# Optimization experiments

Hardware: AMD Instinct MI355X
Metric: run time of the kernel (lower is better)

The kernel has to match this reference:

```python
import jax, jax.numpy as jnp
import numpy as np
from jax import lax

EPS = 1e-5
NBIT = 127.0  # 8-bit symmetric: 2^(8-1)-1

def ste_round(x):
    return x + lax.stop_gradient(jnp.round(x) - x)

def quant_act(x, rng_max):
    # symmetric fake-quant of activations with learned per-cluster range
    s = rng_max / NBIT
    xq = jnp.clip(ste_round(x / s), -NBIT, NBIT) * s
    return xq, s

def fold_bn(w, gamma, beta, mean, var):
    std = jnp.sqrt(var + EPS)
    scale = gamma / std
    w_f = w * scale[:, None, None, None]
    b_f = beta - mean * scale
    return w_f, b_f

def quant_weight(w):
    # per-output-channel symmetric quant
    s = jnp.max(jnp.abs(w), axis=(1, 2, 3), keepdims=True) / NBIT
    wq = jnp.clip(ste_round(w / s), -NBIT, NBIT) * s
    return wq, s.reshape(-1)

def conv(x, w, stride=1, groups=1, pad=0):
    return lax.conv_general_dilated(
        x, w, window_strides=(stride, stride),
        padding=((pad, pad), (pad, pad)),
        dimension_numbers=('NCHW', 'OIHW', 'NCHW'),
        feature_group_count=groups)

def setup_inputs() -> dict:
    key = jax.random.key(0)
    ks = jax.random.split(key, 24)
    B, Cin, H, W = 64, 96, 28, 28
    Cmid, Cout, NC = 576, 96, 4
    d = {}
    d['x'] = jax.random.normal(ks[0], (B, Cin, H, W), dtype=jnp.float32)
    # conv1: 1x1 expansion
    d['w1'] = jax.random.normal(ks[1], (Cmid, Cin, 1, 1), jnp.float32) * 0.1
    d['g1'] = jax.random.uniform(ks[2], (Cmid,), minval=0.5, maxval=1.5)
    d['b1'] = jax.random.normal(ks[3], (Cmid,)) * 0.1
    d['m1'] = jax.random.normal(ks[4], (Cmid,)) * 0.1
    d['v1'] = jax.random.uniform(ks[5], (Cmid,), minval=0.5, maxval=1.5)
    # conv2: 3x3 depthwise
    d['w2'] = jax.random.normal(ks[6], (Cmid, 1, 3, 3), jnp.float32) * 0.1
    d['g2'] = jax.random.uniform(ks[7], (Cmid,), minval=0.5, maxval=1.5)
    d['b2'] = jax.random.normal(ks[8], (Cmid,)) * 0.1
    d['m2'] = jax.random.normal(ks[9], (Cmid,)) * 0.1
    d['v2'] = jax.random.uniform(ks[10], (Cmid,), minval=0.5, maxval=1.5)
    # conv3: 1x1 projection
    d['w3'] = jax.random.normal(ks[11], (Cout, Cmid, 1, 1), jnp.float32) * 0.1
    d['g3'] = jax.random.uniform(ks[12], (Cout,), minval=0.5, maxval=1.5)
    d['b3'] = jax.random.normal(ks[13], (Cout,)) * 0.1
    d['m3'] = jax.random.normal(ks[14], (Cout,)) * 0.1
    d['v3'] = jax.random.uniform(ks[15], (Cout,), minval=0.5, maxval=1.5)
    # per-cluster learned activation ranges for the 4 QuantAct modules
    d['r0'] = jax.random.uniform(ks[16], (NC,), minval=2.0, maxval=8.0)
    d['r1'] = jax.random.uniform(ks[17], (NC,), minval=2.0, maxval=8.0)
    d['r2'] = jax.random.uniform(ks[18], (NC,), minval=2.0, maxval=8.0)
    d['r3'] = jax.random.uniform(ks[19], (NC,), minval=2.0, maxval=8.0)
    d['cluster'] = 2
    return d

def reference(x, w1, g1, b1, m1, v1, w2, g2, b2, m2, v2,
              w3, g3, b3, m3, v3, r0, r1, r2, r3, cluster):
    identity = x  # residual path (in==out, stride==1)
    # QuantAct -> conv1 (BN-folded, per-channel quant) -> ReLU6
    xq, s0 = quant_act(x, r0[cluster])
    w1f, bf1 = fold_bn(w1, g1, b1, m1, v1)
    w1q, ws1 = quant_weight(w1f)
    y = conv(xq, w1q) + bf1[None, :, None, None]
    y = jnp.clip(y, 0.0, 6.0)
    # QuantAct1 -> depthwise conv2 -> ReLU6
    yq, s1 = quant_act(y, r1[cluster])
    w2f, bf2 = fold_bn(w2, g2, b2, m2, v2)
    w2q, ws2 = quant_weight(w2f)
    y = conv(yq, w2q, stride=1, groups=w2.shape[0], pad=1) + bf2[None, :, None, None]
    y = jnp.clip(y, 0.0, 6.0)
    # QuantAct2 -> conv3 projection
    yq, s2 = quant_act(y, r2[cluster])
    w3f, bf3 = fold_bn(w3, g3, b3, m3, v3)
    w3q, ws3 = quant_weight(w3f)
    y = conv(yq, w3q) + bf3[None, :, None, None]
    # residual add, then int32 requant
    y = y + identity
    out, s3 = quant_act(y, r3[cluster])
    return out, s3
```

## Files before the change

kernel.cpp:

```cpp
#include <hip/hip_runtime.h>
#include <cstdint>
#include <cstddef>

typedef int   v4i __attribute__((ext_vector_type(4)));
typedef float v4f __attribute__((ext_vector_type(4)));
typedef unsigned int u32;

constexpr int B_   = 64;
constexpr int CIN  = 96;
constexpr int P_   = 784;
constexpr int CMID = 576;
constexpr int COUT = 96;
constexpr int NOUT = B_ * COUT * P_;
constexpr float NBITF = 127.0f;
constexpr float EPSF  = 1e-5f;
constexpr float MAGICF = 12582912.0f;
constexpr int   BIASI  = 0x4B400000;

constexpr int XB4 = 13 * 8 * 64;

__device__ __forceinline__ int dot3(u32 a, u32 w, int acc) {
#if __has_builtin(__builtin_amdgcn_sdot4)
    return __builtin_amdgcn_sdot4((int)a, (int)w, acc, false);
#else
    return acc + (int)(signed char)(a)        * (int)(signed char)(w)
               + (int)(signed char)(a >> 8)   * (int)(signed char)(w >> 8)
               + (int)(signed char)(a >> 16)  * (int)(signed char)(w >> 16);
#endif
}

__device__ __forceinline__ void tr4(u32 S0, u32 S1, u32 S2, u32 S3, u32 O[4]) {
    u32 u01 = __builtin_amdgcn_perm(S1, S0, 0x05010400u);
    u32 u23 = __builtin_amdgcn_perm(S3, S2, 0x05010400u);
    u32 v01 = __builtin_amdgcn_perm(S1, S0, 0x07030602u);
    u32 v23 = __builtin_amdgcn_perm(S3, S2, 0x07030602u);
    O[0] = __builtin_amdgcn_perm(u23, u01, 0x05040100u);
    O[1] = __builtin_amdgcn_perm(u23, u01, 0x07060302u);
    O[2] = __builtin_amdgcn_perm(v23, v01, 0x05040100u);
    O[3] = __builtin_amdgcn_perm(v23, v01, 0x07060302u);
}

__device__ __forceinline__ u32 pack4(u32 t0, u32 t1, u32 t2, u32 t3) {
    u32 p01 = __builtin_amdgcn_perm(t1, t0, 0x05010400u);
    u32 p23 = __builtin_amdgcn_perm(t3, t2, 0x05010400u);
    return __builtin_amdgcn_perm(p23, p01, 0x05040100u);
}

__global__ __launch_bounds__(256)
void prep_all(const float* __restrict__ x,
              const float* __restrict__ w1, const float* __restrict__ g1,
              const float* __restrict__ b1, const float* __restrict__ m1,
              const float* __restrict__ v1,
              const float* __restrict__ w2, const float* __restrict__ g2,
              const float* __restrict__ b2, const float* __restrict__ m2,
              const float* __restrict__ v2,
              const float* __restrict__ w3, const float* __restrict__ g3,
              const float* __restrict__ b3, const float* __restrict__ m3,
              const float* __restrict__ v3,
              const float* __restrict__ r0, const float* __restrict__ r1,
              const float* __restrict__ r2, const int* __restrict__ cluster,
              u32* __restrict__ x8t2,
              int8_t* __restrict__ w1qp, float2* __restrict__ e1,
              v4i* __restrict__ w2pk,    float2* __restrict__ e2,
              int8_t* __restrict__ w3qp, float2* __restrict__ e3)
{
    __shared__ u32 T[112 * 37];
    int tid = threadIdx.x;
    int c = cluster[0];

    if (blockIdx.x < 448) {
        int pt0 = blockIdx.x % 7, b = blockIdx.x / 7;
        float inv_s0 = NBITF / r0[c];

        for (int i = tid; i < 112 * 8; i += 256) {
            int row = i >> 3, cc = 24 + (i & 7);
            T[row * 37 + cc] = 0u;
        }
        for (int u = tid; u < 24 * 28; u += 256) {
            int pq = u % 28, icq = u / 28;
            int pxb = pt0 * 112 + pq * 4;
            int q[4][4];
            #pragma unroll
            for (int j = 0; j < 4; j++) {
                v4f xv = *(const v4f*)(x + ((size_t)b * CIN + icq * 4 + j) * P_ + pxb);
                #pragma unroll
                for (int i = 0; i < 4; i++)
                    q[j][i] = (int)fminf(fmaxf(rintf(xv[i] * inv_s0), -127.f), 127.f);
            }
            #pragma unroll
            for (int i = 0; i < 4; i++) {
                u32 t0 = __builtin_amdgcn_perm((u32)q[1][i], (u32)q[0][i], 0x00000400u);
                u32 t1 = __builtin_amdgcn_perm((u32)q[3][i], (u32)q[2][i], 0x00000400u);
                T[(pq * 4 + i) * 37 + icq] = __builtin_amdgcn_perm(t1, t0, 0x05040100u);
            }
        }
        __syncthreads();
        u32* gb = x8t2 + (size_t)b * XB4 * 4;
        for (int i = tid; i < 32 * 112; i += 256) {
            int icq = i / 112, pxo = i - icq * 112;
            int px = pt0 * 112 + pxo;
            gb[(((px >> 6) * 8 + (icq >> 2)) * 64 + (px & 63)) * 4 + (icq & 3)] =
                T[pxo * 37 + icq];
        }
        return;
    }

    int lane = tid & 63, wv = tid >> 6;
    int blk = (blockIdx.x - 448) * 4 + wv;

    const float *w, *g, *bb, *mm, *vv;
    int oc, K, which;
    if (blk < CMID)            { which = 0; w = w1; g = g1; bb = b1; mm = m1; vv = v1; oc = blk;            K = CIN;  }
    else if (blk < 2 * CMID)   { which = 1; w = w2; g = g2; bb = b2; mm = m2; vv = v2; oc = blk - CMID;     K = 9;    }
    else                       { which = 2; w = w3; g = g3; bb = b3; mm = m3; vv = v3; oc = blk - 2 * CMID; K = CMID; }

    float scale = g[oc] / sqrtf(vv[oc] + EPSF);

    float mx = 0.f;
    for (int k = lane; k < K; k += 64)
        mx = fmaxf(mx, fabsf(w[oc * K + k] * scale));
    #pragma unroll
    for (int off = 1; off < 64; off <<= 1)
        mx = fmaxf(mx, __shfl_xor(mx, off));

    float s = mx / NBITF;

    int myq = 0;
    for (int k = lane; k < K; k += 64) {
        float wf = w[oc * K + k] * scale;
        float q  = fminf(fmaxf(rintf(wf / s), -127.f), 127.f);
        if (which == 0)      w1qp[oc * 144 + k] = (int8_t)q;
        else if (which == 1) myq = (int)q;
        else                 w3qp[oc * 592 + k] = (int8_t)q;
    }
    if (which == 0 && lane < 12)
        ((u32*)(w1qp + oc * 144))[24 + lane] = 0u;
    if (which == 1) {
        u32 qq[9];
        #pragma unroll
        for (int t = 0; t < 9; t++) qq[t] = (u32)__shfl(myq, t, 64) & 0xffu;
        if (lane == 0) {
            v4i pk;
            pk[0] = (int)(qq[0] | (qq[1] << 8) | (qq[2] << 16));
            pk[1] = (int)(qq[3] | (qq[4] << 8) | (qq[5] << 16));
            pk[2] = (int)(qq[6] | (qq[7] << 8) | (qq[8] << 16));
            pk[3] = 0;
            w2pk[oc] = pk;
        }
    }
    if (lane == 0) {
        float bf = bb[oc] - mm[oc] * scale;
        float s0 = r0[c] / NBITF, s1 = r1[c] / NBITF, s2 = r2[c] / NBITF;
        if (which == 0) {
            float inv_s1 = NBITF / r1[c];
            e1[oc] = make_float2(s0 * s * inv_s1, bf * inv_s1);
        } else if (which == 1) {
            float inv_s2 = NBITF / r2[c];
            e2[oc] = make_float2(s1 * s * inv_s2, bf * inv_s2);
        } else {
            e3[oc] = make_float2(s2 * s, bf);
        }
    }
}

__global__ __launch_bounds__(256)
void conv123(const v4i* __restrict__ x8t2, const v4i* __restrict__ w1q4,
             const float2* __restrict__ e1,
             const v4i* __restrict__ w2pk, const float2* __restrict__ e2,
             const int8_t* __restrict__ w3qp, const float2* __restrict__ e3,
             const float* __restrict__ x,
             const float* __restrict__ r1, const float* __restrict__ r2,
             const float* __restrict__ r3, const int* __restrict__ cluster,
             float* __restrict__ out)
{
    __shared__ v4i xs4[8 * 112];
    __shared__ u32 y1s[4][48 * 29];
    __shared__ u32 y2s[4][48 * 15];
    __shared__ v4i y2c[36 * 57];

    int tid = threadIdx.x, b = blockIdx.y, rt = blockIdx.x;
    int R0 = 2 * rt;
    int W0 = (R0 - 1) * 28;
    int lane = tid & 63, wv = tid >> 6;
    int n = lane & 15, q4 = lane >> 4;

    int   c      = cluster[0];
    int   u1i    = (int)fminf(rintf(6.f * NBITF / r1[c]), 127.f);
    int   u2i    = (int)fminf(rintf(6.f * NBITF / r2[c]), 127.f);
    float s3     = r3[c] / NBITF;
    float inv_s3 = NBITF / r3[c];

    const v4i* xb = x8t2 + (size_t)b * XB4;
    for (int u = tid; u < 896; u += 256) {
        int g = u / 112, pxl = u - g * 112;
        int px = min(max(W0 + pxl, 0), P_ - 1);
        xs4[g * 112 + pxl] = xb[((px >> 6) * 8 + g) * 64 + (px & 63)];
    }
    __syncthreads();

    u32* myY1 = y1s[wv];
    u32* myY2 = y2s[wv];

    for (int ck = 0; ck < 3; ck++) {
        int oc0 = wv * 144 + ck * 48;

        v4i    bw[3][2];
        float2 ee[3];
        #pragma unroll
        for (int jn = 0; jn < 3; jn++) {
            int oc = oc0 + 16 * jn + n;
            bw[jn][0] = w1q4[oc * 9 + q4];
            bw[jn][1] = w1q4[oc * 9 + 4 + q4];
            ee[jn] = e1[oc];
        }
        #pragma unroll
        for (int jm = 0; jm < 7; jm++) {
            v4i af0 = xs4[q4 * 112 + 16 * jm + n];
            v4i af1 = xs4[(4 + q4) * 112 + 16 * jm + n];
            int dw = 4 * jm + q4;
            bool valid = (unsigned)(W0 + 4 * dw) < (unsigned)P_;

            #pragma unroll
            for (int jn = 0; jn < 3; jn++) {
                v4i acc = (v4i){0, 0, 0, 0};
                acc = __builtin_amdgcn_mfma_i32_16x16x64_i8(af0, bw[jn][0], acc, 0, 0, 0);
                acc = __builtin_amdgcn_mfma_i32_16x16x64_i8(af1, bw[jn][1], acc, 0, 0, 0);
                u32 t[4];
                #pragma unroll
                for (int r = 0; r < 4; r++) {
                    float f = fmaf((float)acc[r], ee[jn].x, ee[jn].y) + MAGICF;
                    t[r] = (u32)min(max(__float_as_int(f), BIASI), BIASI + u1i);
                }
                u32 pk = pack4(t[0], t[1], t[2], t[3]);
                myY1[(16 * jn + n) * 29 + dw] = valid ? pk : 0u;
            }
        }

        for (int u = lane; u < 96; u += 64) {
            int chl = u >> 1, orow = u & 1;
            int ch  = oc0 + chl;
            int rb  = chl * 29 + orow * 7;

            v4i wpk = w2pk[ch];
            u32 pk0 = (u32)wpk[0], pk1 = (u32)wpk[1], pk2 = (u32)wpk[2];
            float2 e = e2[ch];

            u32 M0 = 0, M1 = 0, M2 = 0;
            u32 D0 = myY1[rb], D1 = myY1[rb + 7], D2 = myY1[rb + 14];
            #pragma unroll
            for (int xq = 0; xq < 7; xq++) {
                u32 N0, N1, N2;
                if (xq < 6) {
                    N0 = myY1[rb + xq + 1];
                    N1 = myY1[rb + 7 + xq + 1];
                    N2 = myY1[rb + 14 + xq + 1];
                } else { N0 = N1 = N2 = 0u; }

                int a0, a1, a2, a3;
                a0 = dot3(__builtin_amdgcn_alignbyte(D0, M0, 3), pk0, 0);
                a0 = dot3(__builtin_amdgcn_alignbyte(D1, M1, 3), pk1, a0);
                a0 = dot3(__builtin_amdgcn_alignbyte(D2, M2, 3), pk2, a0);
                a1 = dot3(D0, pk0, 0);
                a1 = dot3(D1, pk1, a1);
                a1 = dot3(D2, pk2, a1);
                a2 = dot3(__builtin_amdgcn_alignbyte(N0, D0, 1), pk0, 0);
                a2 = dot3(__builtin_amdgcn_alignbyte(N1, D1, 1), pk1, a2);
                a2 = dot3(__builtin_amdgcn_alignbyte(N2, D2, 1), pk2, a2);
                a3 = dot3(__builtin_amdgcn_alignbyte(N0, D0, 2), pk0, 0);
                a3 = dot3(__builtin_amdgcn_alignbyte(N1, D1, 2), pk1, a3);
                a3 = dot3(__builtin_amdgcn_alignbyte(N2, D2, 2), pk2, a3);

                int aa[4] = {a0, a1, a2, a3};
                u32 tq[4];
                #pragma unroll
                for (int i = 0; i < 4; i++) {
                    float f = fmaf((float)aa[i], e.x, e.y) + MAGICF;
                    tq[i] = (u32)min(max(__float_as_int(f), BIASI), BIASI + u2i);
                }
                myY2[chl * 15 + orow * 7 + xq] = pack4(tq[0], tq[1], tq[2], tq[3]);

                M0 = D0; M1 = D1; M2 = D2;
                D0 = N0; D1 = N1; D2 = N2;
            }
        }

        if (lane < 42) {
            int kgl = lane / 14, d = lane - kgl * 14;
            u32 O[4][4];
            #pragma unroll
            for (int j = 0; j < 4; j++) {
                int cb = (16 * kgl + 4 * j) * 15 + d;
                tr4(myY2[cb], myY2[cb + 15], myY2[cb + 30], myY2[cb + 45], O[j]);
            }
            int kgG = wv * 9 + ck * 3 + kgl;
            #pragma unroll
            for (int i = 0; i < 4; i++)
                y2c[kgG * 57 + 4 * d + i] =
                    (v4i){(int)O[0][i], (int)O[1][i], (int)O[2][i], (int)O[3][i]};
        }
    }
    __syncthreads();

    int pxl = wv * 16 + n;
    int pxc = min(pxl, 55);
    const v4i* w34 = (const v4i*)w3qp;

    v4i acc3[6];
    #pragma unroll
    for (int i = 0; i < 6; i++) acc3[i] = (v4i){0, 0, 0, 0};

    #pragma unroll
    for (int ks = 0; ks < 9; ks++) {
        v4i bfr = y2c[(4 * ks + q4) * 57 + pxc];
        #pragma unroll
        for (int i = 0; i < 6; i++) {
            v4i afr = w34[(i * 16 + n) * 37 + 4 * ks + q4];
            acc3[i] = __builtin_amdgcn_mfma_i32_16x16x64_i8(afr, bfr, acc3[i], 0, 0, 0);
        }
    }

    if (pxl < 56) {
        int px = R0 * 28 + pxl;
        #pragma unroll
        for (int i = 0; i < 6; i++) {
            #pragma unroll
            for (int r = 0; r < 4; r++) {
                int    oc = i * 16 + q4 * 4 + r;
                float2 e  = e3[oc];
                size_t gi = (size_t)(b * COUT + oc) * P_ + px;
                float v  = fmaf((float)acc3[i][r], e.x, e.y) + x[gi];
                float f  = fmaf(v, inv_s3, MAGICF);
                int lvl  = min(max(__float_as_int(f) - BIASI, -127), 127);
                out[gi]  = (float)lvl * s3;
            }
        }
    }
    if (rt == 0 && b == 0 && tid == 0)
        out[NOUT] = s3;
}

extern "C" void kernel_launch(void* const* d_in, const int* in_sizes, int n_in,
                              void* d_out, int out_size, void* d_ws, size_t ws_size,
                              hipStream_t stream)
{
    const float* x  = (const float*)d_in[0];
    const float* w1 = (const float*)d_in[1];
    const float* g1 = (const float*)d_in[2];
    const float* b1 = (const float*)d_in[3];
    const float* m1 = (const float*)d_in[4];
    const float* v1 = (const float*)d_in[5];
    const float* w2 = (const float*)d_in[6];
    const float* g2 = (const float*)d_in[7];
    const float* b2 = (const float*)d_in[8];
    const float* m2 = (const float*)d_in[9];
    const float* v2 = (const float*)d_in[10];
    const float* w3 = (const float*)d_in[11];
    const float* g3 = (const float*)d_in[12];
    const float* b3 = (const float*)d_in[13];
    const float* m3 = (const float*)d_in[14];
    const float* v3 = (const float*)d_in[15];
    const float* r0 = (const float*)d_in[16];
    const float* r1 = (const float*)d_in[17];
    const float* r2 = (const float*)d_in[18];
    const float* r3 = (const float*)d_in[19];
    const int*   cl = (const int*)d_in[20];

    float* out = (float*)d_out;

    char*  ws  = (char*)d_ws;
    size_t off = 0;
    auto carve = [&](size_t bytes) {
        size_t cur = off;
        off = (off + bytes + 255) & ~(size_t)255;
        return (void*)(ws + cur);
    };
    int8_t* w1qp = (int8_t*)carve((size_t)CMID * 144);
    float2* e1   = (float2*)carve((size_t)CMID * 8);
    v4i*    w2pk = (v4i*)carve((size_t)CMID * 16);
    float2* e2   = (float2*)carve((size_t)CMID * 8);
    int8_t* w3qp = (int8_t*)carve((size_t)COUT * 592);
    float2* e3   = (float2*)carve((size_t)COUT * 8);
    u32*    x8t2 = (u32*)carve((size_t)B_ * XB4 * 16);
    (void)ws_size; (void)in_sizes; (void)n_in; (void)out_size;

    prep_all<<<dim3(760), dim3(256), 0, stream>>>(
        x, w1, g1, b1, m1, v1, w2, g2, b2, m2, v2, w3, g3, b3, m3, v3,
        r0, r1, r2, cl, x8t2,
        w1qp, e1, w2pk, e2, w3qp, e3);

    conv123<<<dim3(14, B_), dim3(256), 0, stream>>>(
        (const v4i*)x8t2, (const v4i*)w1qp, e1, w2pk, e2, w3qp, e3,
        x, r1, r2, r3, cl, out);
}
```

Before: 164.6 us.

## Process 16-channel chunks and read input fragments directly from global memory

The fused conv kernel drops the shared-memory staging of the input tile and has each lane load its MFMA A-fragments straight from global (L1/L2) memory inside the channel loop. It also cuts the per-iteration output-channel chunk from 48 to 16, so each warp runs 9 iterations instead of 3 and the y1/y2 scratch buffers shrink. This lowers LDS use and register pressure, which may let more blocks fit per CU. The cost is that the input tile is re-read from global memory 9 times per warp instead of once per block. The depthwise and transpose stages also use fewer active lanes per iteration.

```diff
diff --git a/kernel.cpp b/kernel.cpp
--- a/kernel.cpp
+++ b/kernel.cpp
@@ -164,18 +164,17 @@
 }
 
 __global__ __launch_bounds__(256)
-void conv123(const v4i* __restrict__ x8t2, const v4i* __restrict__ w1q4,
-             const float2* __restrict__ e1,
-             const v4i* __restrict__ w2pk, const float2* __restrict__ e2,
-             const int8_t* __restrict__ w3qp, const float2* __restrict__ e3,
-             const float* __restrict__ x,
-             const float* __restrict__ r1, const float* __restrict__ r2,
-             const float* __restrict__ r3, const int* __restrict__ cluster,
-             float* __restrict__ out)
+void conv123b(const v4i* __restrict__ x8t2, const v4i* __restrict__ w1q4,
+              const float2* __restrict__ e1,
+              const v4i* __restrict__ w2pk, const float2* __restrict__ e2,
+              const int8_t* __restrict__ w3qp, const float2* __restrict__ e3,
+              const float* __restrict__ x,
+              const float* __restrict__ r1, const float* __restrict__ r2,
+              const float* __restrict__ r3, const int* __restrict__ cluster,
+              float* __restrict__ out)
 {
-    __shared__ v4i xs4[8 * 112];
-    __shared__ u32 y1s[4][48 * 29];
-    __shared__ u32 y2s[4][48 * 15];
+    __shared__ u32 y1s[4][16 * 29];
+    __shared__ u32 y2s[4][16 * 15];
     __shared__ v4i y2c[36 * 57];
 
     int tid = threadIdx.x, b = blockIdx.y, rt = blockIdx.x;
@@ -191,53 +190,47 @@
     float inv_s3 = NBITF / r3[c];
 
     const v4i* xb = x8t2 + (size_t)b * XB4;
-    for (int u = tid; u < 896; u += 256) {
-        int g = u / 112, pxl = u - g * 112;
-        int px = min(max(W0 + pxl, 0), P_ - 1);
-        xs4[g * 112 + pxl] = xb[((px >> 6) * 8 + g) * 64 + (px & 63)];
-    }
-    __syncthreads();
+    int pb[7];
+    #pragma unroll
+    for (int jm = 0; jm < 7; jm++) {
+        int px = min(max(W0 + 16 * jm + n, 0), P_ - 1);
+        pb[jm] = (px >> 6) * 512 + (px & 63);
+    }
 
     u32* myY1 = y1s[wv];
     u32* myY2 = y2s[wv];
 
-    for (int ck = 0; ck < 3; ck++) {
-        int oc0 = wv * 144 + ck * 48;
-
-        v4i    bw[3][2];
-        float2 ee[3];
-        #pragma unroll
-        for (int jn = 0; jn < 3; jn++) {
-            int oc = oc0 + 16 * jn + n;
-            bw[jn][0] = w1q4[oc * 9 + q4];
-            bw[jn][1] = w1q4[oc * 9 + 4 + q4];
-            ee[jn] = e1[oc];
-        }
+    for (int ck = 0; ck < 9; ck++) {
+        int oc0 = wv * 144 + ck * 16;
+
+        int    oc  = oc0 + n;
+        v4i    bw0 = w1q4[oc * 9 + q4];
+        v4i    bw1 = w1q4[oc * 9 + 4 + q4];
+        float2 ee  = e1[oc];
+
         #pragma unroll
         for (int jm = 0; jm < 7; jm++) {
-            v4i af0 = xs4[q4 * 112 + 16 * jm + n];
-            v4i af1 = xs4[(4 + q4) * 112 + 16 * jm + n];
+            v4i af0 = xb[pb[jm] + q4 * 64];
+            v4i af1 = xb[pb[jm] + (4 + q4) * 64];
             int dw = 4 * jm + q4;
             bool valid = (unsigned)(W0 + 4 * dw) < (unsigned)P_;
 
-            #pragma unroll
-            for (int jn = 0; jn < 3; jn++) {
-                v4i acc = (v4i){0, 0, 0, 0};
-                acc = __builtin_amdgcn_mfma_i32_16x16x64_i8(af0, bw[jn][0], acc, 0, 0, 0);
-                acc = __builtin_amdgcn_mfma_i32_16x16x64_i8(af1, bw[jn][1], acc, 0, 0, 0);
-                u32 t[4];
-                #pragma unroll
-                for (int r = 0; r < 4; r++) {
-                    float f = fmaf((float)acc[r], ee[jn].x, ee[jn].y) + MAGICF;
-                    t[r] = (u32)min(max(__float_as_int(f), BIASI), BIASI + u1i);
-                }
-                u32 pk = pack4(t[0], t[1], t[2], t[3]);
-                myY1[(16 * jn + n) * 29 + dw] = valid ? pk : 0u;
-            }
-        }
-
-        for (int u = lane; u < 96; u += 64) {
-            int chl = u >> 1, orow = u & 1;
+            v4i acc = (v4i){0, 0, 0, 0};
+            acc = __builtin_amdgcn_mfma_i32_16x16x64_i8(af0, bw0, acc, 0, 0, 0);
+            acc = __builtin_amdgcn_mfma_i32_16x16x64_i8(af1, bw1, acc, 0, 0, 0);
+
+            u32 t[4];
+            #pragma unroll
+            for (int r = 0; r < 4; r++) {
+                float f = fmaf((float)acc[r], ee.x, ee.y) + MAGICF;
+                t[r] = (u32)min(max(__float_as_int(f), BIASI), BIASI + u1i);
+            }
+            u32 pk = pack4(t[0], t[1], t[2], t[3]);
+            myY1[n * 29 + dw] = valid ? pk : 0u;
+        }
+
+        if (lane < 32) {
+            int chl = lane >> 1, orow = lane & 1;
             int ch  = oc0 + chl;
             int rb  = chl * 29 + orow * 7;
 
@@ -284,15 +277,15 @@
             }
         }
 
-        if (lane < 42) {
-            int kgl = lane / 14, d = lane - kgl * 14;
+        if (lane < 14) {
+            int d = lane;
             u32 O[4][4];
             #pragma unroll
             for (int j = 0; j < 4; j++) {
-                int cb = (16 * kgl + 4 * j) * 15 + d;
+                int cb = (4 * j) * 15 + d;
                 tr4(myY2[cb], myY2[cb + 15], myY2[cb + 30], myY2[cb + 45], O[j]);
             }
-            int kgG = wv * 9 + ck * 3 + kgl;
+            int kgG = wv * 9 + ck;
             #pragma unroll
             for (int i = 0; i < 4; i++)
                 y2c[kgG * 57 + 4 * d + i] =
@@ -388,7 +381,7 @@
         r0, r1, r2, cl, x8t2,
         w1qp, e1, w2pk, e2, w3qp, e3);
 
-    conv123<<<dim3(14, B_), dim3(256), 0, stream>>>(
+    conv123b<<<dim3(14, B_), dim3(256), 0, stream>>>(
         (const v4i*)x8t2, (const v4i*)w1qp, e1, w2pk, e2, w3qp, e3,
         x, r1, r2, r3, cl, out);
 }
```

New measurement: 169.4 us. 1.03x slower.

## Cut LDS footprint: read x fragments from global, alias y2 into y1 buffer

Applied to the files above, without the earlier changes.

Drops the shared-memory staging of the input tile, so MFMA A-fragments are loaded straight from global (L2-cached) memory with precomputed per-lane offsets, which also removes a block barrier. The depthwise output is written back into unused columns of the per-wave y1 buffer instead of a separate y2 buffer, and the y2c stride shrinks from 57 to 56. Together these lower LDS use per block, aiming for more resident blocks per CU. The costs are repeated global loads of x fragments across the three channel chunks and possible LDS bank conflicts from the unpadded stride.

```diff
diff --git a/kernel.cpp b/kernel.cpp
--- a/kernel.cpp
+++ b/kernel.cpp
@@ -164,19 +164,17 @@
 }
 
 __global__ __launch_bounds__(256)
-void conv123(const v4i* __restrict__ x8t2, const v4i* __restrict__ w1q4,
-             const float2* __restrict__ e1,
-             const v4i* __restrict__ w2pk, const float2* __restrict__ e2,
-             const int8_t* __restrict__ w3qp, const float2* __restrict__ e3,
-             const float* __restrict__ x,
-             const float* __restrict__ r1, const float* __restrict__ r2,
-             const float* __restrict__ r3, const int* __restrict__ cluster,
-             float* __restrict__ out)
+void conv123c(const v4i* __restrict__ x8t2, const v4i* __restrict__ w1q4,
+              const float2* __restrict__ e1,
+              const v4i* __restrict__ w2pk, const float2* __restrict__ e2,
+              const int8_t* __restrict__ w3qp, const float2* __restrict__ e3,
+              const float* __restrict__ x,
+              const float* __restrict__ r1, const float* __restrict__ r2,
+              const float* __restrict__ r3, const int* __restrict__ cluster,
+              float* __restrict__ out)
 {
-    __shared__ v4i xs4[8 * 112];
     __shared__ u32 y1s[4][48 * 29];
-    __shared__ u32 y2s[4][48 * 15];
-    __shared__ v4i y2c[36 * 57];
+    __shared__ v4i y2c[36 * 56];
 
     int tid = threadIdx.x, b = blockIdx.y, rt = blockIdx.x;
     int R0 = 2 * rt;
@@ -191,15 +189,14 @@
     float inv_s3 = NBITF / r3[c];
 
     const v4i* xb = x8t2 + (size_t)b * XB4;
-    for (int u = tid; u < 896; u += 256) {
-        int g = u / 112, pxl = u - g * 112;
-        int px = min(max(W0 + pxl, 0), P_ - 1);
-        xs4[g * 112 + pxl] = xb[((px >> 6) * 8 + g) * 64 + (px & 63)];
-    }
-    __syncthreads();
+    int pb[7];
+    #pragma unroll
+    for (int jm = 0; jm < 7; jm++) {
+        int px = min(max(W0 + 16 * jm + n, 0), P_ - 1);
+        pb[jm] = (px >> 6) * 512 + (px & 63);
+    }
 
     u32* myY1 = y1s[wv];
-    u32* myY2 = y2s[wv];
 
     for (int ck = 0; ck < 3; ck++) {
         int oc0 = wv * 144 + ck * 48;
@@ -215,8 +212,8 @@
         }
         #pragma unroll
         for (int jm = 0; jm < 7; jm++) {
-            v4i af0 = xs4[q4 * 112 + 16 * jm + n];
-            v4i af1 = xs4[(4 + q4) * 112 + 16 * jm + n];
+            v4i af0 = xb[pb[jm] + q4 * 64];
+            v4i af1 = xb[pb[jm] + (4 + q4) * 64];
             int dw = 4 * jm + q4;
             bool valid = (unsigned)(W0 + 4 * dw) < (unsigned)P_;
 
@@ -240,6 +237,7 @@
             int chl = u >> 1, orow = u & 1;
             int ch  = oc0 + chl;
             int rb  = chl * 29 + orow * 7;
+            int wb  = chl * 29 + orow * 21;
 
             v4i wpk = w2pk[ch];
             u32 pk0 = (u32)wpk[0], pk1 = (u32)wpk[1], pk2 = (u32)wpk[2];
@@ -277,7 +275,7 @@
                     float f = fmaf((float)aa[i], e.x, e.y) + MAGICF;
                     tq[i] = (u32)min(max(__float_as_int(f), BIASI), BIASI + u2i);
                 }
-                myY2[chl * 15 + orow * 7 + xq] = pack4(tq[0], tq[1], tq[2], tq[3]);
+                myY1[wb + xq] = pack4(tq[0], tq[1], tq[2], tq[3]);
 
                 M0 = D0; M1 = D1; M2 = D2;
                 D0 = N0; D1 = N1; D2 = N2;
@@ -286,16 +284,18 @@
 
         if (lane < 42) {
             int kgl = lane / 14, d = lane - kgl * 14;
+            int off = d + ((d >= 7) ? 14 : 0);
             u32 O[4][4];
             #pragma unroll
             for (int j = 0; j < 4; j++) {
-                int cb = (16 * kgl + 4 * j) * 15 + d;
-                tr4(myY2[cb], myY2[cb + 15], myY2[cb + 30], myY2[cb + 45], O[j]);
+                int ch0 = 16 * kgl + 4 * j;
+                tr4(myY1[(ch0 + 0) * 29 + off], myY1[(ch0 + 1) * 29 + off],
+                    myY1[(ch0 + 2) * 29 + off], myY1[(ch0 + 3) * 29 + off], O[j]);
             }
             int kgG = wv * 9 + ck * 3 + kgl;
             #pragma unroll
             for (int i = 0; i < 4; i++)
-                y2c[kgG * 57 + 4 * d + i] =
+                y2c[kgG * 56 + 4 * d + i] =
                     (v4i){(int)O[0][i], (int)O[1][i], (int)O[2][i], (int)O[3][i]};
         }
     }
@@ -311,7 +311,7 @@
 
     #pragma unroll
     for (int ks = 0; ks < 9; ks++) {
-        v4i bfr = y2c[(4 * ks + q4) * 57 + pxc];
+        v4i bfr = y2c[(4 * ks + q4) * 56 + pxc];
         #pragma unroll
         for (int i = 0; i < 6; i++) {
             v4i afr = w34[(i * 16 + n) * 37 + 4 * ks + q4];
@@ -388,7 +388,7 @@
         r0, r1, r2, cl, x8t2,
         w1qp, e1, w2pk, e2, w3qp, e3);
 
-    conv123<<<dim3(14, B_), dim3(256), 0, stream>>>(
+    conv123c<<<dim3(14, B_), dim3(256), 0, stream>>>(
         (const v4i*)x8t2, (const v4i*)w1qp, e1, w2pk, e2, w3qp, e3,
         x, r1, r2, r3, cl, out);
 }
```

Result: no change. 164.2 us (-0.2%).
